# Optimization experiments

Hardware: AMD Instinct MI355X
Metric: run time of the kernel (lower is better)

The kernel has to match this reference:

```python
import jax, jax.numpy as jnp
import numpy as np

CHANNELS = 8
RADIUS = 2


def setup_inputs() -> dict:
    key = jax.random.key(0)
    k1, k2, k3 = jax.random.split(key, 3)
    x = jax.random.normal(k1, (4, CHANNELS + 1, 1024, 1024), dtype=jnp.float32)
    rand = jax.random.uniform(k2, (4, CHANNELS, 1024, 1024), dtype=jnp.float32)
    dropout_rand = jax.random.uniform(k3, (1024, 1024), dtype=jnp.float32)
    return {"x": x, "rand": rand, "dropout_rand": dropout_rand}


def reference(x, rand, dropout_rand):
    # x: [B, C+1, H, W]; spins in first C channels, inverse-temperature b in last.
    s = x[:, :CHANNELS]          # [B, C, H, W]
    b = x[:, -1:]                # [B, 1, H, W]

    # Cross-shaped stencil conv with all-ones weights shared across channels
    # (weight shape [1, C, Rk, Rk]): equivalent to summing over channels, then
    # summing circular rolls along the row and column of the cross. The circular
    # pad + valid conv is exactly a circular roll, so no padding is materialized.
    sc = s.sum(axis=1)           # [B, H, W]
    Js = sc  # center tap (weight 1, counted once)
    for d in range(1, RADIUS + 1):
        Js = Js + jnp.roll(sc, d, axis=-2) + jnp.roll(sc, -d, axis=-2)
        Js = Js + jnp.roll(sc, d, axis=-1) + jnp.roll(sc, -d, axis=-1)
    Js = Js[:, None]             # [B, 1, H, W], broadcasts over channels

    delta_e = 2.0 * s * Js       # [B, C, H, W]
    p = jnp.where(delta_e <= 0, jnp.ones_like(s), jnp.exp(-delta_e * b))
    dropout_mask = (dropout_rand > 0.5)[None, None]   # [1, 1, H, W]
    flip = 1.0 - 2.0 * ((rand < p) & dropout_mask).astype(s.dtype)
    return jnp.concatenate([s * flip, b], axis=1)
```

## Files before the change

### kernel.cpp

```cpp
#include <hip/hip_runtime.h>
#include <math.h>


#define NB 4
#define NC 8
#define HH 1024
#define WW 1024
#define PIX (HH * WW)
#define STEPS 4

typedef float f32x4 __attribute__((ext_vector_type(4)));

__global__ __launch_bounds__(256) void sc_kernel(const float* __restrict__ x,
                                                 float* __restrict__ sc) {
    int tid = blockIdx.x * 256 + threadIdx.x;
    int n   = tid >> 18;
    int g   = tid & ((PIX / 4) - 1);
    const float* base = x + (size_t)n * 9 * PIX + (size_t)g * 4;
    f32x4 s = *reinterpret_cast<const f32x4*>(base);
#pragma unroll
    for (int c = 1; c < NC; ++c) {
        f32x4 t = *reinterpret_cast<const f32x4*>(base + (size_t)c * PIX);
        s = s + t;
    }
    *reinterpret_cast<f32x4*>(sc + (size_t)n * PIX + (size_t)g * 4) = s;
}

__global__ __launch_bounds__(256) void ising_kernel(const float* __restrict__ x,
                                                    const float* __restrict__ rnd,
                                                    const float* __restrict__ dr,
                                                    const float* __restrict__ sc,
                                                    float* __restrict__ out) {
    int bid = blockIdx.x;
    int n   = bid / (HH / STEPS);
    int y0  = (bid % (HH / STEPS)) * STEPS;
    int xc  = threadIdx.x << 2;
    int xA  = (xc - 4) & (WW - 1);
    int xC  = (xc + 4) & (WW - 1);

    const float* scn = sc + (size_t)n * PIX;
#define LDSC(row, col) (*reinterpret_cast<const f32x4*>(scn + ((((row) & (HH - 1))) << 10) + (col)))

    f32x4 m2 = LDSC(y0 - 2, xc);
    f32x4 m1 = LDSC(y0 - 1, xc);
    f32x4 ce = LDSC(y0,     xc);
    f32x4 p1 = LDSC(y0 + 1, xc);
    f32x4 p2 = LDSC(y0 + 2, xc);

    const float* xs = x   + (size_t)n * 9  * PIX + (y0 << 10) + xc;
    const float* rs = rnd + (size_t)n * NC * PIX + (y0 << 10) + xc;
    float*       os = out + (size_t)n * 9  * PIX + (y0 << 10) + xc;
    const float* dp = dr  + (y0 << 10) + xc;

#pragma unroll
    for (int st = 0; st < STEPS; ++st) {
        int y = y0 + st;
        f32x4 rA = LDSC(y, xA);
        f32x4 rC = LDSC(y, xC);
        f32x4 bv = __builtin_nontemporal_load(
                       reinterpret_cast<const f32x4*>(xs + (size_t)NC * PIX));
        f32x4 dv = *reinterpret_cast<const f32x4*>(dp);

        float Js[4];
#pragma unroll
        for (int i = 0; i < 4; ++i) {
            float vx1m = (i == 0) ? rA[3] : ce[i - 1];
            float vx1p = (i == 3) ? rC[0] : ce[i + 1];
            float vx2m = (i < 2) ? rA[2 + i] : ce[i - 2];
            float vx2p = (i < 2) ? ce[i + 2] : rC[i - 2];
            float j = ce[i];
            j = j + m1[i]; j = j + p1[i];
            j = j + vx1m;  j = j + vx1p;
            j = j + m2[i]; j = j + p2[i];
            j = j + vx2m;  j = j + vx2p;
            Js[i] = j;
        }
        bool dm[4];
#pragma unroll
        for (int i = 0; i < 4; ++i) dm[i] = dv[i] > 0.5f;

#pragma unroll
        for (int c = 0; c < NC; ++c) {
            f32x4 sv = __builtin_nontemporal_load(
                           reinterpret_cast<const f32x4*>(xs + (size_t)c * PIX));
            f32x4 rv = __builtin_nontemporal_load(
                           reinterpret_cast<const f32x4*>(rs + (size_t)c * PIX));
            float de[4], arg[4];
            bool fl[4], und[4];
            bool anyund = false;
#pragma unroll
            for (int i = 0; i < 4; ++i) {
                de[i]  = (2.0f * sv[i]) * Js[i];
                arg[i] = (-de[i]) * bv[i];
                float pa   = __expf(arg[i]);
                float band = pa * 4.0e-5f;
                bool  l = rv[i] < pa - band;
                bool  h = rv[i] > pa + band;
                fl[i]  = l;
                und[i] = (de[i] > 0.0f) && !l && !h;
                anyund = anyund || und[i];
            }
            f32x4 o;
            if (__any(anyund)) {
#pragma unroll
                for (int i = 0; i < 4; ++i) {
                    bool take;
                    if (de[i] <= 0.0f)  take = true;
                    else if (und[i])    take = rv[i] < (float)exp((double)arg[i]);
                    else                take = fl[i];
                    o[i] = (take && dm[i]) ? -sv[i] : sv[i];
                }
            } else {
#pragma unroll
                for (int i = 0; i < 4; ++i) {
                    bool take = (de[i] <= 0.0f) || fl[i];
                    o[i] = (take && dm[i]) ? -sv[i] : sv[i];
                }
            }
            __builtin_nontemporal_store(
                o, reinterpret_cast<f32x4*>(os + (size_t)c * PIX));
        }
        __builtin_nontemporal_store(
            bv, reinterpret_cast<f32x4*>(os + (size_t)NC * PIX));

        if (st < STEPS - 1) {
            m2 = m1; m1 = ce; ce = p1; p1 = p2;
            p2 = LDSC(y + 3, xc);
            xs += WW; rs += WW; os += WW; dp += WW;
        }
    }
#undef LDSC
}

extern "C" void kernel_launch(void* const* d_in, const int* in_sizes, int n_in,
                              void* d_out, int out_size, void* d_ws, size_t ws_size,
                              hipStream_t stream) {
    const float* x   = (const float*)d_in[0];
    const float* rnd = (const float*)d_in[1];
    const float* dr  = (const float*)d_in[2];
    float* out = (float*)d_out;
    float* sc  = (float*)d_ws;

    sc_kernel<<<NB * PIX / 4 / 256, 256, 0, stream>>>(x, sc);
    ising_kernel<<<NB * HH / STEPS, 256, 0, stream>>>(x, rnd, dr, sc, out);
}
```

Measured before the change: 106.4 us.

## Fuse channel-sum and Ising update into one kernel with LDS ring buffer

Drops the separate channel-sum kernel and its global workspace. Each block now computes per-row channel sums on the fly into an 8-row shared-memory ring buffer, and keeps each row's spin vectors in registers so x is loaded once for both the sum and the flip. The point is to remove the workspace round trip, the second pass over x and one kernel launch. In exchange, each block re-reads 4 halo rows of all channels, adds a barrier per row step, raises register pressure from three rows of 8-channel vectors, and changes rows per block from 4 to 8 with an interleaved block order.

```diff
diff --git a/kernel.cpp b/kernel.cpp
--- a/kernel.cpp
+++ b/kernel.cpp
@@ -7,67 +7,100 @@
 #define HH 1024
 #define WW 1024
 #define PIX (HH * WW)
-#define STEPS 4
+#define S 8
+#define NBLK (NB * (HH / S))
 
 typedef float f32x4 __attribute__((ext_vector_type(4)));
 
-__global__ __launch_bounds__(256) void sc_kernel(const float* __restrict__ x,
-                                                 float* __restrict__ sc) {
-    int tid = blockIdx.x * 256 + threadIdx.x;
-    int n   = tid >> 18;
-    int g   = tid & ((PIX / 4) - 1);
-    const float* base = x + (size_t)n * 9 * PIX + (size_t)g * 4;
-    f32x4 s = *reinterpret_cast<const f32x4*>(base);
-#pragma unroll
-    for (int c = 1; c < NC; ++c) {
-        f32x4 t = *reinterpret_cast<const f32x4*>(base + (size_t)c * PIX);
-        s = s + t;
-    }
-    *reinterpret_cast<f32x4*>(sc + (size_t)n * PIX + (size_t)g * 4) = s;
-}
+__global__ __launch_bounds__(256) void ising_fused(const float* __restrict__ x,
+                                                   const float* __restrict__ rnd,
+                                                   const float* __restrict__ dr,
+                                                   float* __restrict__ out) {
+    __shared__ float scb[8][WW];
 
-__global__ __launch_bounds__(256) void ising_kernel(const float* __restrict__ x,
-                                                    const float* __restrict__ rnd,
-                                                    const float* __restrict__ dr,
-                                                    const float* __restrict__ sc,
-                                                    float* __restrict__ out) {
-    int bid = blockIdx.x;
-    int n   = bid / (HH / STEPS);
-    int y0  = (bid % (HH / STEPS)) * STEPS;
-    int xc  = threadIdx.x << 2;
-    int xA  = (xc - 4) & (WW - 1);
-    int xC  = (xc + 4) & (WW - 1);
+    int bid     = blockIdx.x;
+    int logical = (bid & 7) * (NBLK / 8) + (bid >> 3);
+    int n       = logical / (HH / S);
+    int y0      = (logical % (HH / S)) * S;
+    int xc      = (int)(threadIdx.x << 2);
+    int xA      = (xc - 4) & (WW - 1);
+    int xC      = (xc + 4) & (WW - 1);
 
-    const float* scn = sc + (size_t)n * PIX;
-#define LDSC(row, col) (*reinterpret_cast<const f32x4*>(scn + ((((row) & (HH - 1))) << 10) + (col)))
+    const float* xn = x   + (size_t)n * 9  * PIX;
+    const float* rn = rnd + (size_t)n * NC * PIX;
+    float*       on = out + (size_t)n * 9  * PIX;
 
-    f32x4 m2 = LDSC(y0 - 2, xc);
-    f32x4 m1 = LDSC(y0 - 1, xc);
-    f32x4 ce = LDSC(y0,     xc);
-    f32x4 p1 = LDSC(y0 + 1, xc);
-    f32x4 p2 = LDSC(y0 + 2, xc);
-
-    const float* xs = x   + (size_t)n * 9  * PIX + (y0 << 10) + xc;
-    const float* rs = rnd + (size_t)n * NC * PIX + (y0 << 10) + xc;
-    float*       os = out + (size_t)n * 9  * PIX + (y0 << 10) + xc;
-    const float* dp = dr  + (y0 << 10) + xc;
+    f32x4 svA[NC], svB[NC], svC[NC];
 
 #pragma unroll
-    for (int st = 0; st < STEPS; ++st) {
-        int y = y0 + st;
-        f32x4 rA = LDSC(y, xA);
-        f32x4 rC = LDSC(y, xC);
-        f32x4 bv = __builtin_nontemporal_load(
-                       reinterpret_cast<const f32x4*>(xs + (size_t)NC * PIX));
-        f32x4 dv = *reinterpret_cast<const f32x4*>(dp);
+    for (int h = 0; h < 2; ++h) {
+        int yr = (y0 - 2 + h) & (HH - 1);
+        const float* base = xn + ((size_t)yr << 10) + xc;
+        f32x4 s = *reinterpret_cast<const f32x4*>(base);
+#pragma unroll
+        for (int c = 1; c < NC; ++c)
+            s = s + *reinterpret_cast<const f32x4*>(base + (size_t)c * PIX);
+        *reinterpret_cast<f32x4*>(&scb[(y0 - 2 + h) & 7][xc]) = s;
+    }
+    {
+        const float* base = xn + ((size_t)y0 << 10) + xc;
+#pragma unroll
+        for (int c = 0; c < NC; ++c)
+            svA[c] = *reinterpret_cast<const f32x4*>(base + (size_t)c * PIX);
+        f32x4 s = svA[0];
+#pragma unroll
+        for (int c = 1; c < NC; ++c) s = s + svA[c];
+        *reinterpret_cast<f32x4*>(&scb[y0 & 7][xc]) = s;
+    }
+    {
+        int yr = (y0 + 1) & (HH - 1);
+        const float* base = xn + ((size_t)yr << 10) + xc;
+#pragma unroll
+        for (int c = 0; c < NC; ++c)
+            svB[c] = *reinterpret_cast<const f32x4*>(base + (size_t)c * PIX);
+        f32x4 s = svB[0];
+#pragma unroll
+        for (int c = 1; c < NC; ++c) s = s + svB[c];
+        *reinterpret_cast<f32x4*>(&scb[(y0 + 1) & 7][xc]) = s;
+    }
+
+#pragma unroll
+    for (int st = 0; st < S; ++st) {
+        int y  = y0 + st;
+        int yw = y & (HH - 1);
+
+        {
+            int yr = (y + 2) & (HH - 1);
+            const float* base = xn + ((size_t)yr << 10) + xc;
+#pragma unroll
+            for (int c = 0; c < NC; ++c)
+                svC[c] = *reinterpret_cast<const f32x4*>(base + (size_t)c * PIX);
+            f32x4 s = svC[0];
+#pragma unroll
+            for (int c = 1; c < NC; ++c) s = s + svC[c];
+            *reinterpret_cast<f32x4*>(&scb[(y + 2) & 7][xc]) = s;
+        }
+        f32x4 bv = __builtin_nontemporal_load(reinterpret_cast<const f32x4*>(
+                       xn + (size_t)NC * PIX + ((size_t)yw << 10) + xc));
+        f32x4 dv = *reinterpret_cast<const f32x4*>(dr + ((size_t)yw << 10) + xc);
+
+        __syncthreads();
+
+        f32x4 m2  = *reinterpret_cast<const f32x4*>(&scb[(y - 2) & 7][xc]);
+        f32x4 m1  = *reinterpret_cast<const f32x4*>(&scb[(y - 1) & 7][xc]);
+        f32x4 ce  = *reinterpret_cast<const f32x4*>(&scb[ y      & 7][xc]);
+        f32x4 p1  = *reinterpret_cast<const f32x4*>(&scb[(y + 1) & 7][xc]);
+        f32x4 p2  = *reinterpret_cast<const f32x4*>(&scb[(y + 2) & 7][xc]);
+        f32x4 rAq = *reinterpret_cast<const f32x4*>(&scb[ y      & 7][xA]);
+        f32x4 rCq = *reinterpret_cast<const f32x4*>(&scb[ y      & 7][xC]);
 
         float Js[4];
 #pragma unroll
         for (int i = 0; i < 4; ++i) {
-            float vx1m = (i == 0) ? rA[3] : ce[i - 1];
-            float vx1p = (i == 3) ? rC[0] : ce[i + 1];
-            float vx2m = (i < 2) ? rA[2 + i] : ce[i - 2];
-            float vx2p = (i < 2) ? ce[i + 2] : rC[i - 2];
+            float vx1m = (i == 0) ? rAq[3] : ce[i - 1];
+            float vx1p = (i == 3) ? rCq[0] : ce[i + 1];
+            float vx2m = (i < 2) ? rAq[2 + i] : ce[i - 2];
+            float vx2p = (i < 2) ? ce[i + 2] : rCq[i - 2];
             float j = ce[i];
             j = j + m1[i]; j = j + p1[i];
             j = j + vx1m;  j = j + vx1p;
@@ -79,12 +112,14 @@
 #pragma unroll
         for (int i = 0; i < 4; ++i) dm[i] = dv[i] > 0.5f;
 
+        const float* rbase = rn + ((size_t)yw << 10) + xc;
+        float*       obase = on + ((size_t)yw << 10) + xc;
+
 #pragma unroll
         for (int c = 0; c < NC; ++c) {
-            f32x4 sv = __builtin_nontemporal_load(
-                           reinterpret_cast<const f32x4*>(xs + (size_t)c * PIX));
+            f32x4 sv = svA[c];
             f32x4 rv = __builtin_nontemporal_load(
-                           reinterpret_cast<const f32x4*>(rs + (size_t)c * PIX));
+                           reinterpret_cast<const f32x4*>(rbase + (size_t)c * PIX));
             float de[4], arg[4];
             bool fl[4], und[4];
             bool anyund = false;
@@ -118,18 +153,14 @@
                 }
             }
             __builtin_nontemporal_store(
-                o, reinterpret_cast<f32x4*>(os + (size_t)c * PIX));
+                o, reinterpret_cast<f32x4*>(obase + (size_t)c * PIX));
         }
         __builtin_nontemporal_store(
-            bv, reinterpret_cast<f32x4*>(os + (size_t)NC * PIX));
+            bv, reinterpret_cast<f32x4*>(obase + (size_t)NC * PIX));
 
-        if (st < STEPS - 1) {
-            m2 = m1; m1 = ce; ce = p1; p1 = p2;
-            p2 = LDSC(y + 3, xc);
-            xs += WW; rs += WW; os += WW; dp += WW;
-        }
+#pragma unroll
+        for (int c = 0; c < NC; ++c) { svA[c] = svB[c]; svB[c] = svC[c]; }
     }
-#undef LDSC
 }
 
 extern "C" void kernel_launch(void* const* d_in, const int* in_sizes, int n_in,
@@ -139,8 +170,7 @@
     const float* rnd = (const float*)d_in[1];
     const float* dr  = (const float*)d_in[2];
     float* out = (float*)d_out;
-    float* sc  = (float*)d_ws;
+    (void)d_ws; (void)ws_size;
 
-    sc_kernel<<<NB * PIX / 4 / 256, 256, 0, stream>>>(x, sc);
-    ising_kernel<<<NB * HH / STEPS, 256, 0, stream>>>(x, rnd, dr, sc, out);
+    ising_fused<<<NBLK, 256, 0, stream>>>(x, rnd, dr, out);
 }
```

Result: no change. 107.6 us (+1.2%).
